# Kernel tuning notes

Measured on AMD Instinct MI355X. Metric: run time of the kernel, lower is better.

Reference implementation:

```python
import jax, jax.numpy as jnp
import numpy as np

D = 64        # dense voxel grid extent per axis
C = 256       # planes
R = 128       # planes // reduction
N = 100000    # number of occupied (unique) sparse voxels
K = 7         # max-pool kernel size
PAD = 3       # (K-1)//2, stride-1 'same' window


def setup_inputs() -> dict:
    key = jax.random.key(0)
    k1, k2, k3, k4 = jax.random.split(key, 4)
    feats = jax.random.normal(k1, (N, C), dtype=jnp.float32)
    # unique sparse coordinates in [0, D)^3 (MinkowskiEngine coords are unique)
    lin = jax.random.permutation(k2, D * D * D)[:N]
    coords = jnp.stack(jnp.unravel_index(lin, (D, D, D)), axis=-1).astype(jnp.int32)
    # 1x1 sparse convs == per-point linear layers (ME default bias=False)
    W1 = jax.random.normal(k3, (C, R), dtype=jnp.float32) * (1.0 / np.sqrt(C))
    W2 = jax.random.normal(k4, (R, C), dtype=jnp.float32) * (1.0 / np.sqrt(R))
    return {"feats": feats, "coords": coords, "W1": W1, "W2": W2}


def reference(feats, coords, W1, W2):
    neg_inf = jnp.array(-jnp.inf, dtype=feats.dtype)
    ix, iy, iz = coords[:, 0], coords[:, 1], coords[:, 2]
    # scatter sparse features into a dense grid; empty voxels = -inf so they
    grid = jnp.full((D, D, D, C), neg_inf, dtype=feats.dtype).at[ix, iy, iz].set(feats)
    # MinkowskiMaxPooling(kernel_size=7, stride=1): max over [-3,3]^3 window
    pooled = jax.lax.reduce_window(
        grid, neg_inf, jax.lax.max,
        window_dimensions=(K, K, K, 1),
        window_strides=(1, 1, 1, 1),
        padding=[(PAD, PAD), (PAD, PAD), (PAD, PAD), (0, 0)],
    )
    y = pooled[ix, iy, iz]  # [N, C], gather back to sparse points
    # fc: 1x1 conv -> ReLU -> 1x1 conv -> sigmoid (per-point MLP)
    y = jax.nn.sigmoid(jax.nn.relu(y @ W1) @ W2)
    return feats * y
```

## Files before the change

### kernel.cpp

```cpp
#include <hip/hip_runtime.h>
#include <hip/hip_bf16.h>

#define GD 64
#define GC 256

typedef unsigned short u16;
typedef unsigned int u32;
typedef short bf16x8 __attribute__((ext_vector_type(8)));
typedef float f32x4 __attribute__((ext_vector_type(4)));

__device__ __forceinline__ u16 f2bf_rne(float f) {
    u32 u = __builtin_bit_cast(u32, f);
    u = (u + 0x7FFFu + ((u >> 16) & 1u)) >> 16;
    return (u16)u;
}

__global__ __launch_bounds__(256) void init_grid(uint4* __restrict__ g, int n16) {
    int i = blockIdx.x * 256 + threadIdx.x;
    if (i < n16) {
        uint4 v;
        v.x = v.y = v.z = v.w = 0xFF80FF80u;
        g[i] = v;
    }
}

__global__ __launch_bounds__(256) void scatter_feats(const float* __restrict__ feats,
        const int* __restrict__ coords, u16* __restrict__ grid, int n) {
    int t = blockIdx.x * 256 + threadIdx.x;
    int i = t >> 5;
    if (i >= n) return;
    int c8 = (t & 31) << 3;
    int ix = coords[3 * i], iy = coords[3 * i + 1], iz = coords[3 * i + 2];
    size_t cell = (size_t)((ix * GD + iy) * GD + iz);
    const float4* src = (const float4*)(feats + (size_t)i * GC + c8);
    float4 a = src[0], b = src[1];
    u32 p0 = (u32)f2bf_rne(a.x) | ((u32)f2bf_rne(a.y) << 16);
    u32 p1 = (u32)f2bf_rne(a.z) | ((u32)f2bf_rne(a.w) << 16);
    u32 p2 = (u32)f2bf_rne(b.x) | ((u32)f2bf_rne(b.y) << 16);
    u32 p3 = (u32)f2bf_rne(b.z) | ((u32)f2bf_rne(b.w) << 16);
    uint4 v = make_uint4(p0, p1, p2, p3);
    *(uint4*)(grid + cell * GC + c8) = v;
}

__global__ __launch_bounds__(256) void prep_weights(const float* __restrict__ W1,
        const float* __restrict__ W2, u16* __restrict__ img1, u16* __restrict__ img2) {
    int t = blockIdx.x * 256 + threadIdx.x;
    if (t < 32768) {
        int h = t >> 14, nn = (t >> 8) & 63, chunk = (t >> 3) & 31, j = t & 7;
        int k = chunk * 8 + j;
        img1[(h << 14) + nn * 256 + (((chunk ^ (nn & 7)) << 3) | j)] =
            f2bf_rne(W1[k * 128 + h * 64 + nn]);
    } else {
        int t2 = t - 32768;
        int h = t2 >> 14, nn = (t2 >> 7) & 127, chunk = (t2 >> 3) & 15, j = t2 & 7;
        int k = chunk * 8 + j;
        img2[(h << 14) + nn * 128 + (((chunk ^ (nn & 7)) << 3) | j)] =
            f2bf_rne(W2[k * 256 + h * 128 + nn]);
    }
}

__device__ __forceinline__ void unpack8(uint4 r, float* w) {
    u32 v[4] = {r.x, r.y, r.z, r.w};
#pragma unroll
    for (int i = 0; i < 4; i++) {
        w[2 * i]     = __builtin_bit_cast(float, v[i] << 16);
        w[2 * i + 1] = __builtin_bit_cast(float, v[i] & 0xFFFF0000u);
    }
}

__global__ __launch_bounds__(256) void pool_pass_v(u16* __restrict__ grid,
        int mulA, int mulB, int strideCell) {
    int chunk = threadIdx.x & 31;
    int L = blockIdx.x * 8 + (threadIdx.x >> 5);
    int a = L >> 6, b = L & 63;
    size_t baseEl = ((size_t)a * mulA + (size_t)b * mulB) * GC + chunk * 8;
    size_t stepEl = (size_t)strideCell * GC;
    u16* p = grid + baseEl;

    float win[7][8];
#pragma unroll
    for (int s = 0; s < 7; s++)
#pragma unroll
        for (int c = 0; c < 8; c++) win[s][c] = -INFINITY;

#pragma unroll
    for (int t = 0; t < 3; t++) {
        uint4 r = *(const uint4*)(p + (size_t)t * stepEl);
        unpack8(r, win[t + 3]);
    }

#pragma unroll
    for (int z = 0; z < 64; z++) {
        int slot = (z + 6) % 7;
        if (z + 3 < 64) {
            uint4 r = *(const uint4*)(p + (size_t)(z + 3) * stepEl);
            unpack8(r, win[slot]);
        } else {
#pragma unroll
            for (int c = 0; c < 8; c++) win[slot][c] = -INFINITY;
        }
        u32 q[4];
#pragma unroll
        for (int i = 0; i < 4; i++) {
            u32 halves[2];
#pragma unroll
            for (int hh = 0; hh < 2; hh++) {
                int c = 2 * i + hh;
                float m01 = fmaxf(win[0][c], win[1][c]);
                float m23 = fmaxf(win[2][c], win[3][c]);
                float m45 = fmaxf(win[4][c], win[5][c]);
                float m = fmaxf(fmaxf(m01, m23), fmaxf(m45, win[6][c]));
                halves[hh] = __builtin_bit_cast(u32, m);
            }
            q[i] = (halves[0] >> 16) | (halves[1] & 0xFFFF0000u);
        }
        *(uint4*)(p + (size_t)z * stepEl) = make_uint4(q[0], q[1], q[2], q[3]);
    }
}

__global__ __launch_bounds__(256, 4) void gemm1_kernel(const u16* __restrict__ grid,
        const int* __restrict__ coords, const u16* __restrict__ img1,
        u16* __restrict__ H, int n, int nrb) {
    __shared__ __align__(16) u16 w1t[64 * 256];
    int h = blockIdx.x >= nrb;
    int rb = blockIdx.x - (h ? nrb : 0);
    int tid = threadIdx.x;

    const uint4* src = (const uint4*)(img1 + (h << 14));
    uint4* dst = (uint4*)w1t;
#pragma unroll
    for (int i = 0; i < 8; i++) dst[i * 256 + tid] = src[i * 256 + tid];

    int wave = tid >> 6, lane = tid & 63, m16 = lane & 15, quad = lane >> 4;
    int row_a = rb * 64 + wave * 16 + m16;
    int ra = min(row_a, n - 1);
    int ix = coords[3 * ra], iy = coords[3 * ra + 1], iz = coords[3 * ra + 2];
    const u16* yrow = grid + (size_t)((ix * GD + iy) * GD + iz) * GC;
    bf16x8 afr[8];
#pragma unroll
    for (int kk = 0; kk < 8; kk++)
        afr[kk] = *(const bf16x8*)(yrow + kk * 32 + quad * 8);
    __syncthreads();

    f32x4 acc[4];
#pragma unroll
    for (int t = 0; t < 4; t++) acc[t] = (f32x4){0.f, 0.f, 0.f, 0.f};
#pragma unroll
    for (int kk = 0; kk < 8; kk++) {
        int chunk = kk * 4 + quad;
#pragma unroll
        for (int t = 0; t < 4; t++) {
            int r = t * 16 + m16;
            bf16x8 b = *(const bf16x8*)&w1t[r * 256 + ((chunk ^ (r & 7)) << 3)];
            acc[t] = __builtin_amdgcn_mfma_f32_16x16x32_bf16(afr[kk], b, acc[t], 0, 0, 0);
        }
    }
    __syncthreads();

    u16* hbuf = w1t;
#pragma unroll
    for (int t = 0; t < 4; t++) {
        int col = t * 16 + m16;
        int c8 = col >> 3, j = col & 7;
#pragma unroll
        for (int rr = 0; rr < 4; rr++) {
            int row_l = wave * 16 + quad * 4 + rr;
            float hv = fmaxf(acc[t][rr], 0.0f);
            hbuf[row_l * 64 + (((c8 ^ (row_l & 7)) << 3) | j)] = f2bf_rne(hv);
        }
    }
    __syncthreads();
#pragma unroll
    for (int i = 0; i < 2; i++) {
        int cid = i * 256 + tid;
        int row_l = cid >> 3, c8 = cid & 7;
        int grow = rb * 64 + row_l;
        if (grow < n) {
            bf16x8 v = *(const bf16x8*)&hbuf[row_l * 64 + ((c8 ^ (row_l & 7)) << 3)];
            *(bf16x8*)&H[(size_t)grow * 128 + h * 64 + c8 * 8] = v;
        }
    }
}

__global__ __launch_bounds__(256, 4) void gemm2_kernel(const u16* __restrict__ H,
        const u16* __restrict__ img2, const float* __restrict__ feats,
        float* __restrict__ out, int n, int nrb) {
    __shared__ __align__(16) char smem[64 * 140 * 4];
    u16* w2t = (u16*)smem;
    float* zbuf = (float*)smem;
    int h = blockIdx.x >= nrb;
    int rb = blockIdx.x - (h ? nrb : 0);
    int tid = threadIdx.x;

    const uint4* src = (const uint4*)(img2 + (h << 14));
    uint4* dst = (uint4*)w2t;
#pragma unroll
    for (int i = 0; i < 8; i++) dst[i * 256 + tid] = src[i * 256 + tid];

    int wave = tid >> 6, lane = tid & 63, m16 = lane & 15, quad = lane >> 4;
    int row_a = rb * 64 + wave * 16 + m16;
    int ra = min(row_a, n - 1);
    const u16* hrow = H + (size_t)ra * 128;
    bf16x8 afr[4];
#pragma unroll
    for (int kk = 0; kk < 4; kk++)
        afr[kk] = *(const bf16x8*)(hrow + kk * 32 + quad * 8);
    __syncthreads();

    f32x4 acc[8];
#pragma unroll
    for (int t = 0; t < 8; t++) acc[t] = (f32x4){0.f, 0.f, 0.f, 0.f};
#pragma unroll
    for (int kk = 0; kk < 4; kk++) {
        int chunk = kk * 4 + quad;
#pragma unroll
        for (int t = 0; t < 8; t++) {
            int nn = t * 16 + m16;
            bf16x8 b = *(const bf16x8*)&w2t[nn * 128 + ((chunk ^ (nn & 7)) << 3)];
            acc[t] = __builtin_amdgcn_mfma_f32_16x16x32_bf16(afr[kk], b, acc[t], 0, 0, 0);
        }
    }
    __syncthreads();

#pragma unroll
    for (int t = 0; t < 8; t++) {
        int col = t * 16 + m16;
#pragma unroll
        for (int rr = 0; rr < 4; rr++) {
            int row_l = wave * 16 + quad * 4 + rr;
            zbuf[row_l * 140 + col] = acc[t][rr];
        }
    }
    __syncthreads();
#pragma unroll
    for (int i = 0; i < 8; i++) {
        int f = i * 256 + tid;
        int row_l = f >> 5, c4 = f & 31;
        int grow = rb * 64 + row_l;
        if (grow < n) {
            f32x4 z = *(const f32x4*)&zbuf[row_l * 140 + c4 * 4];
            size_t o = (size_t)grow * 256 + h * 128 + c4 * 4;
            f32x4 ft = *(const f32x4*)&feats[o];
            f32x4 r;
#pragma unroll
            for (int c = 0; c < 4; c++)
                r[c] = ft[c] / (1.0f + __expf(-z[c]));
            *(f32x4*)&out[o] = r;
        }
    }
}

extern "C" void kernel_launch(void* const* d_in, const int* in_sizes, int n_in,
                              void* d_out, int out_size, void* d_ws, size_t ws_size,
                              hipStream_t stream) {
    const float* feats = (const float*)d_in[0];
    const int* coords = (const int*)d_in[1];
    const float* W1 = (const float*)d_in[2];
    const float* W2 = (const float*)d_in[3];
    float* out = (float*)d_out;

    int n = in_sizes[1] / 3;

    size_t grid_bytes = (size_t)GD * GD * GD * GC * 2;
    u16* grid = (u16*)d_ws;
    u16* H = (u16*)((char*)d_ws + grid_bytes);
    u16* img1 = (u16*)((char*)d_ws + grid_bytes + (size_t)n * 128 * 2);
    u16* img2 = img1 + 32768;

    int n16 = (int)(grid_bytes / 16);
    init_grid<<<n16 / 256, 256, 0, stream>>>((uint4*)d_ws, n16);

    prep_weights<<<256, 256, 0, stream>>>(W1, W2, img1, img2);

    scatter_feats<<<(n * 32 + 255) / 256, 256, 0, stream>>>(feats, coords, grid, n);

    pool_pass_v<<<512, 256, 0, stream>>>(grid, GD * GD, GD, 1);
    pool_pass_v<<<512, 256, 0, stream>>>(grid, GD * GD, 1, GD);
    pool_pass_v<<<512, 256, 0, stream>>>(grid, GD, 1, GD * GD);

    int nrb = (n + 63) / 64;
    gemm1_kernel<<<2 * nrb, 256, 0, stream>>>(grid, coords, img1, H, n, nrb);
    gemm2_kernel<<<2 * nrb, 256, 0, stream>>>(H, img2, feats, out, n, nrb);
}
```

Measured before the change: 380.8 us.

## Replace dense grid init with occupancy map and fuse z/y pooling passes

Drops the full 134MB grid fill by tracking occupancy in an int map (-1 empty) and skipping reads of empty cells during the z pass. The z and y pooling passes are fused into one kernel that does the z sliding window in registers and the y window through a double-buffered shared tile. The final x pass writes pooled rows only for occupied cells into a compact per-point buffer, so gemm1 reads contiguously instead of gathering through coords. The cost is an extra map buffer and a block barrier per z step.

```diff
diff --git a/kernel.cpp b/kernel.cpp
--- a/kernel.cpp
+++ b/kernel.cpp
@@ -15,31 +15,168 @@
     return (u16)u;
 }
 
-__global__ __launch_bounds__(256) void init_grid(uint4* __restrict__ g, int n16) {
+__device__ __forceinline__ void unpack8(uint4 r, float* w) {
+    u32 v[4] = {r.x, r.y, r.z, r.w};
+#pragma unroll
+    for (int i = 0; i < 4; i++) {
+        w[2 * i]     = __builtin_bit_cast(float, v[i] << 16);
+        w[2 * i + 1] = __builtin_bit_cast(float, v[i] & 0xFFFF0000u);
+    }
+}
+
+__global__ __launch_bounds__(256) void init_map(uint4* __restrict__ m) {
     int i = blockIdx.x * 256 + threadIdx.x;
-    if (i < n16) {
-        uint4 v;
-        v.x = v.y = v.z = v.w = 0xFF80FF80u;
-        g[i] = v;
-    }
+    uint4 v;
+    v.x = v.y = v.z = v.w = 0xFFFFFFFFu;
+    m[i] = v;
 }
 
 __global__ __launch_bounds__(256) void scatter_feats(const float* __restrict__ feats,
-        const int* __restrict__ coords, u16* __restrict__ grid, int n) {
+        const int* __restrict__ coords, u16* __restrict__ grid,
+        int* __restrict__ map, int n) {
     int t = blockIdx.x * 256 + threadIdx.x;
     int i = t >> 5;
     if (i >= n) return;
     int c8 = (t & 31) << 3;
     int ix = coords[3 * i], iy = coords[3 * i + 1], iz = coords[3 * i + 2];
-    size_t cell = (size_t)((ix * GD + iy) * GD + iz);
+    int cell = (ix * GD + iy) * GD + iz;
+    if ((t & 31) == 0) map[cell] = i;
     const float4* src = (const float4*)(feats + (size_t)i * GC + c8);
     float4 a = src[0], b = src[1];
     u32 p0 = (u32)f2bf_rne(a.x) | ((u32)f2bf_rne(a.y) << 16);
     u32 p1 = (u32)f2bf_rne(a.z) | ((u32)f2bf_rne(a.w) << 16);
     u32 p2 = (u32)f2bf_rne(b.x) | ((u32)f2bf_rne(b.y) << 16);
     u32 p3 = (u32)f2bf_rne(b.z) | ((u32)f2bf_rne(b.w) << 16);
-    uint4 v = make_uint4(p0, p1, p2, p3);
-    *(uint4*)(grid + cell * GC + c8) = v;
+    *(uint4*)(grid + (size_t)cell * GC + c8) = make_uint4(p0, p1, p2, p3);
+}
+
+__global__ __launch_bounds__(512) void pool_zy(u16* __restrict__ grid,
+        const int* __restrict__ map) {
+    int x = blockIdx.x >> 2, cg = blockIdx.x & 3;
+    int y = threadIdx.x >> 3, c = threadIdx.x & 7;
+    int chunk = cg * 8 + c;
+    const int* mrow = map + (x * GD + y) * GD;
+    u16* p = grid + (size_t)((x * GD + y) * GD) * GC + chunk * 8;
+
+    __shared__ __align__(16) u16 zp[2][64][8][8];
+
+    float win[7][8];
+#pragma unroll
+    for (int s = 0; s < 7; s++)
+#pragma unroll
+        for (int cc = 0; cc < 8; cc++) win[s][cc] = -INFINITY;
+
+#pragma unroll
+    for (int t = 0; t < 3; t++) {
+        if (mrow[t] >= 0) {
+            uint4 r = *(const uint4*)(p + (size_t)t * GC);
+            unpack8(r, win[t + 3]);
+        }
+    }
+
+#pragma unroll
+    for (int z = 0; z < 64; z++) {
+        int slot = (z + 6) % 7;
+        if (z + 3 < 64 && mrow[z + 3] >= 0) {
+            uint4 r = *(const uint4*)(p + (size_t)(z + 3) * GC);
+            unpack8(r, win[slot]);
+        } else {
+#pragma unroll
+            for (int cc = 0; cc < 8; cc++) win[slot][cc] = -INFINITY;
+        }
+
+        float mz[8];
+#pragma unroll
+        for (int cc = 0; cc < 8; cc++) {
+            float m01 = fmaxf(win[0][cc], win[1][cc]);
+            float m23 = fmaxf(win[2][cc], win[3][cc]);
+            float m45 = fmaxf(win[4][cc], win[5][cc]);
+            mz[cc] = fmaxf(fmaxf(m01, m23), fmaxf(m45, win[6][cc]));
+        }
+        u32 q[4];
+#pragma unroll
+        for (int iq = 0; iq < 4; iq++) {
+            u32 h0 = __builtin_bit_cast(u32, mz[2 * iq]);
+            u32 h1 = __builtin_bit_cast(u32, mz[2 * iq + 1]);
+            q[iq] = (h0 >> 16) | (h1 & 0xFFFF0000u);
+        }
+        *(uint4*)&zp[z & 1][y][c][0] = make_uint4(q[0], q[1], q[2], q[3]);
+        __syncthreads();
+
+#pragma unroll
+        for (int dy = -3; dy <= 3; dy++) {
+            if (dy == 0) continue;
+            int yy = y + dy;
+            if (yy >= 0 && yy < 64) {
+                uint4 r = *(const uint4*)&zp[z & 1][yy][c][0];
+                float w[8];
+                unpack8(r, w);
+#pragma unroll
+                for (int cc = 0; cc < 8; cc++) mz[cc] = fmaxf(mz[cc], w[cc]);
+            }
+        }
+        u32 o[4];
+#pragma unroll
+        for (int iq = 0; iq < 4; iq++) {
+            u32 h0 = __builtin_bit_cast(u32, mz[2 * iq]);
+            u32 h1 = __builtin_bit_cast(u32, mz[2 * iq + 1]);
+            o[iq] = (h0 >> 16) | (h1 & 0xFFFF0000u);
+        }
+        *(uint4*)(p + (size_t)z * GC) = make_uint4(o[0], o[1], o[2], o[3]);
+    }
+}
+
+__global__ __launch_bounds__(256) void pool_x_compact(const u16* __restrict__ grid,
+        const int* __restrict__ map, u16* __restrict__ P) {
+    int chunk = threadIdx.x & 31;
+    int L = blockIdx.x * 8 + (threadIdx.x >> 5);
+    int y = L >> 6, z = L & 63;
+    int cellBase = y * GD + z;
+    const u16* p = grid + (size_t)cellBase * GC + chunk * 8;
+    size_t stepEl = (size_t)(GD * GD) * GC;
+
+    float win[7][8];
+#pragma unroll
+    for (int s = 0; s < 7; s++)
+#pragma unroll
+        for (int cc = 0; cc < 8; cc++) win[s][cc] = -INFINITY;
+
+#pragma unroll
+    for (int t = 0; t < 3; t++) {
+        uint4 r = *(const uint4*)(p + (size_t)t * stepEl);
+        unpack8(r, win[t + 3]);
+    }
+
+#pragma unroll
+    for (int x = 0; x < 64; x++) {
+        int slot = (x + 6) % 7;
+        if (x + 3 < 64) {
+            uint4 r = *(const uint4*)(p + (size_t)(x + 3) * stepEl);
+            unpack8(r, win[slot]);
+        } else {
+#pragma unroll
+            for (int cc = 0; cc < 8; cc++) win[slot][cc] = -INFINITY;
+        }
+        int mi = map[cellBase + x * GD * GD];
+        if (mi >= 0) {
+            u32 q[4];
+#pragma unroll
+            for (int iq = 0; iq < 4; iq++) {
+                u32 halves[2];
+#pragma unroll
+                for (int hh = 0; hh < 2; hh++) {
+                    int cc = 2 * iq + hh;
+                    float m01 = fmaxf(win[0][cc], win[1][cc]);
+                    float m23 = fmaxf(win[2][cc], win[3][cc]);
+                    float m45 = fmaxf(win[4][cc], win[5][cc]);
+                    float m = fmaxf(fmaxf(m01, m23), fmaxf(m45, win[6][cc]));
+                    halves[hh] = __builtin_bit_cast(u32, m);
+                }
+                q[iq] = (halves[0] >> 16) | (halves[1] & 0xFFFF0000u);
+            }
+            *(uint4*)(P + (size_t)mi * GC + chunk * 8) = make_uint4(q[0], q[1], q[2], q[3]);
+        }
+    }
 }
 
 __global__ __launch_bounds__(256) void prep_weights(const float* __restrict__ W1,
@@ -59,68 +196,8 @@
     }
 }
 
-__device__ __forceinline__ void unpack8(uint4 r, float* w) {
-    u32 v[4] = {r.x, r.y, r.z, r.w};
-#pragma unroll
-    for (int i = 0; i < 4; i++) {
-        w[2 * i]     = __builtin_bit_cast(float, v[i] << 16);
-        w[2 * i + 1] = __builtin_bit_cast(float, v[i] & 0xFFFF0000u);
-    }
-}
-
-__global__ __launch_bounds__(256) void pool_pass_v(u16* __restrict__ grid,
-        int mulA, int mulB, int strideCell) {
-    int chunk = threadIdx.x & 31;
-    int L = blockIdx.x * 8 + (threadIdx.x >> 5);
-    int a = L >> 6, b = L & 63;
-    size_t baseEl = ((size_t)a * mulA + (size_t)b * mulB) * GC + chunk * 8;
-    size_t stepEl = (size_t)strideCell * GC;
-    u16* p = grid + baseEl;
-
-    float win[7][8];
-#pragma unroll
-    for (int s = 0; s < 7; s++)
-#pragma unroll
-        for (int c = 0; c < 8; c++) win[s][c] = -INFINITY;
-
-#pragma unroll
-    for (int t = 0; t < 3; t++) {
-        uint4 r = *(const uint4*)(p + (size_t)t * stepEl);
-        unpack8(r, win[t + 3]);
-    }
-
-#pragma unroll
-    for (int z = 0; z < 64; z++) {
-        int slot = (z + 6) % 7;
-        if (z + 3 < 64) {
-            uint4 r = *(const uint4*)(p + (size_t)(z + 3) * stepEl);
-            unpack8(r, win[slot]);
-        } else {
-#pragma unroll
-            for (int c = 0; c < 8; c++) win[slot][c] = -INFINITY;
-        }
-        u32 q[4];
-#pragma unroll
-        for (int i = 0; i < 4; i++) {
-            u32 halves[2];
-#pragma unroll
-            for (int hh = 0; hh < 2; hh++) {
-                int c = 2 * i + hh;
-                float m01 = fmaxf(win[0][c], win[1][c]);
-                float m23 = fmaxf(win[2][c], win[3][c]);
-                float m45 = fmaxf(win[4][c], win[5][c]);
-                float m = fmaxf(fmaxf(m01, m23), fmaxf(m45, win[6][c]));
-                halves[hh] = __builtin_bit_cast(u32, m);
-            }
-            q[i] = (halves[0] >> 16) | (halves[1] & 0xFFFF0000u);
-        }
-        *(uint4*)(p + (size_t)z * stepEl) = make_uint4(q[0], q[1], q[2], q[3]);
-    }
-}
-
-__global__ __launch_bounds__(256, 4) void gemm1_kernel(const u16* __restrict__ grid,
-        const int* __restrict__ coords, const u16* __restrict__ img1,
-        u16* __restrict__ H, int n, int nrb) {
+__global__ __launch_bounds__(256, 4) void gemm1_kernel(const u16* __restrict__ P,
+        const u16* __restrict__ img1, u16* __restrict__ H, int n, int nrb) {
     __shared__ __align__(16) u16 w1t[64 * 256];
     int h = blockIdx.x >= nrb;
     int rb = blockIdx.x - (h ? nrb : 0);
@@ -134,8 +211,7 @@
     int wave = tid >> 6, lane = tid & 63, m16 = lane & 15, quad = lane >> 4;
     int row_a = rb * 64 + wave * 16 + m16;
     int ra = min(row_a, n - 1);
-    int ix = coords[3 * ra], iy = coords[3 * ra + 1], iz = coords[3 * ra + 2];
-    const u16* yrow = grid + (size_t)((ix * GD + iy) * GD + iz) * GC;
+    const u16* yrow = P + (size_t)ra * GC;
     bf16x8 afr[8];
 #pragma unroll
     for (int kk = 0; kk < 8; kk++)
@@ -262,23 +338,23 @@
     int n = in_sizes[1] / 3;
 
     size_t grid_bytes = (size_t)GD * GD * GD * GC * 2;
+    size_t P_bytes = (size_t)n * GC * 2;
+    size_t H_bytes = (size_t)n * 128 * 2;
     u16* grid = (u16*)d_ws;
-    u16* H = (u16*)((char*)d_ws + grid_bytes);
-    u16* img1 = (u16*)((char*)d_ws + grid_bytes + (size_t)n * 128 * 2);
+    u16* P = (u16*)((char*)d_ws + grid_bytes);
+    u16* H = (u16*)((char*)d_ws + grid_bytes + P_bytes);
+    int* map = (int*)((char*)d_ws + grid_bytes + P_bytes + H_bytes);
+    u16* img1 = (u16*)((char*)map + (size_t)GD * GD * GD * 4);
     u16* img2 = img1 + 32768;
 
-    int n16 = (int)(grid_bytes / 16);
-    init_grid<<<n16 / 256, 256, 0, stream>>>((uint4*)d_ws, n16);
-
+    init_map<<<256, 256, 0, stream>>>((uint4*)map);
     prep_weights<<<256, 256, 0, stream>>>(W1, W2, img1, img2);
-
-    scatter_feats<<<(n * 32 + 255) / 256, 256, 0, stream>>>(feats, coords, grid, n);
-
-    pool_pass_v<<<512, 256, 0, stream>>>(grid, GD * GD, GD, 1);
-    pool_pass_v<<<512, 256, 0, stream>>>(grid, GD * GD, 1, GD);
-    pool_pass_v<<<512, 256, 0, stream>>>(grid, GD, 1, GD * GD);
+    scatter_feats<<<(n * 32 + 255) / 256, 256, 0, stream>>>(feats, coords, grid, map, n);
+
+    pool_zy<<<256, 512, 0, stream>>>(grid, map);
+    pool_x_compact<<<512, 256, 0, stream>>>(grid, map, P);
 
     int nrb = (n + 63) / 64;
-    gemm1_kernel<<<2 * nrb, 256, 0, stream>>>(grid, coords, img1, H, n, nrb);
+    gemm1_kernel<<<2 * nrb, 256, 0, stream>>>(P, img1, H, n, nrb);
     gemm2_kernel<<<2 * nrb, 256, 0, stream>>>(H, img2, feats, out, n, nrb);
 }
```

After: 623.1 us. 63.6% more time.

## Replace dense grid init and scatter with index map; fuse gather and compaction into pool passes

Applied to the files above, without the earlier changes.

Drops the dense grid fill and the feature scatter. A 64^3 index map is built instead, and the first pooling pass (z) reads features straight through that map. The y pass goes out-of-place into a second grid, and the x pass writes results only for occupied voxels into a compact [N,C] buffer that gemm1 reads contiguously. Each pooling thread now computes 4 outputs from a 10-wide window with high parallelism, where before each thread walked a 64-long serial sweep. This removes a full-grid memory write and the scattered gather, at the cost of doubling workspace usage.

```diff
diff --git a/kernel.cpp b/kernel.cpp
--- a/kernel.cpp
+++ b/kernel.cpp
@@ -15,31 +15,191 @@
     return (u16)u;
 }
 
-__global__ __launch_bounds__(256) void init_grid(uint4* __restrict__ g, int n16) {
+__device__ __forceinline__ float bfval(float f) {
+    u32 u = __builtin_bit_cast(u32, f);
+    u = (u + 0x7FFFu + ((u >> 16) & 1u)) & 0xFFFF0000u;
+    return __builtin_bit_cast(float, u);
+}
+
+__device__ __forceinline__ void unpack8(uint4 r, float* w) {
+    u32 v[4] = {r.x, r.y, r.z, r.w};
+#pragma unroll
+    for (int i = 0; i < 4; i++) {
+        w[2 * i]     = __builtin_bit_cast(float, v[i] << 16);
+        w[2 * i + 1] = __builtin_bit_cast(float, v[i] & 0xFFFF0000u);
+    }
+}
+
+__global__ __launch_bounds__(256) void init_map(uint4* __restrict__ m) {
     int i = blockIdx.x * 256 + threadIdx.x;
-    if (i < n16) {
-        uint4 v;
-        v.x = v.y = v.z = v.w = 0xFF80FF80u;
-        g[i] = v;
-    }
-}
-
-__global__ __launch_bounds__(256) void scatter_feats(const float* __restrict__ feats,
-        const int* __restrict__ coords, u16* __restrict__ grid, int n) {
-    int t = blockIdx.x * 256 + threadIdx.x;
-    int i = t >> 5;
-    if (i >= n) return;
-    int c8 = (t & 31) << 3;
-    int ix = coords[3 * i], iy = coords[3 * i + 1], iz = coords[3 * i + 2];
-    size_t cell = (size_t)((ix * GD + iy) * GD + iz);
-    const float4* src = (const float4*)(feats + (size_t)i * GC + c8);
-    float4 a = src[0], b = src[1];
-    u32 p0 = (u32)f2bf_rne(a.x) | ((u32)f2bf_rne(a.y) << 16);
-    u32 p1 = (u32)f2bf_rne(a.z) | ((u32)f2bf_rne(a.w) << 16);
-    u32 p2 = (u32)f2bf_rne(b.x) | ((u32)f2bf_rne(b.y) << 16);
-    u32 p3 = (u32)f2bf_rne(b.z) | ((u32)f2bf_rne(b.w) << 16);
-    uint4 v = make_uint4(p0, p1, p2, p3);
-    *(uint4*)(grid + cell * GC + c8) = v;
+    uint4 v;
+    v.x = v.y = v.z = v.w = 0xFFFFFFFFu;
+    m[i] = v;
+}
+
+__global__ __launch_bounds__(256) void build_map(const int* __restrict__ coords,
+        int* __restrict__ map, int n) {
+    int i = blockIdx.x * 256 + threadIdx.x;
+    if (i < n) {
+        int ix = coords[3 * i], iy = coords[3 * i + 1], iz = coords[3 * i + 2];
+        map[(ix * GD + iy) * GD + iz] = i;
+    }
+}
+
+__device__ __forceinline__ void max4pack(const float (&v)[10][8], u32 (&q)[4][4]) {
+#pragma unroll
+    for (int i = 0; i < 4; i++) {
+        u32 h[4][2];
+#pragma unroll
+        for (int hh = 0; hh < 2; hh++) {
+            int ch = 2 * i + hh;
+            float p0 = fmaxf(v[0][ch], v[1][ch]);
+            float p2 = fmaxf(v[2][ch], v[3][ch]);
+            float p4 = fmaxf(v[4][ch], v[5][ch]);
+            float p6 = fmaxf(v[6][ch], v[7][ch]);
+            float p8 = fmaxf(v[8][ch], v[9][ch]);
+            float o0 = fmaxf(fmaxf(p0, p2), fmaxf(p4, v[6][ch]));
+            float o1 = fmaxf(fmaxf(v[1][ch], p2), fmaxf(p4, p6));
+            float o2 = fmaxf(fmaxf(p2, p4), fmaxf(p6, v[8][ch]));
+            float o3 = fmaxf(fmaxf(v[3][ch], p4), fmaxf(p6, p8));
+            h[0][hh] = __builtin_bit_cast(u32, o0);
+            h[1][hh] = __builtin_bit_cast(u32, o1);
+            h[2][hh] = __builtin_bit_cast(u32, o2);
+            h[3][hh] = __builtin_bit_cast(u32, o3);
+        }
+#pragma unroll
+        for (int d = 0; d < 4; d++)
+            q[d][i] = (h[d][0] >> 16) | (h[d][1] & 0xFFFF0000u);
+    }
+}
+
+__global__ __launch_bounds__(256, 3) void pool_z_gather(const float* __restrict__ feats,
+        const int* __restrict__ map, u16* __restrict__ grid) {
+    int lane = threadIdx.x & 31;
+    int gid = blockIdx.x * 8 + (threadIdx.x >> 5);
+    int L = gid >> 4;
+    int a0 = (gid & 15) << 2;
+    const int* mrow = map + L * GD;
+    const float* fb = feats + lane * 8;
+    u16* po = grid + ((size_t)L * GD + a0) * GC + lane * 8;
+
+    int mi[10];
+#pragma unroll
+    for (int i = 0; i < 10; i++) {
+        int w = a0 - 3 + i;
+        int wc = min(max(w, 0), 63);
+        int m = mrow[wc];
+        mi[i] = ((unsigned)w < 64u) ? m : -1;
+    }
+
+    float4 fa[10], fbb[10];
+#pragma unroll
+    for (int i = 0; i < 10; i++) {
+        const float4* f4 = (const float4*)(fb + (size_t)max(mi[i], 0) * GC);
+        fa[i] = f4[0];
+        fbb[i] = f4[1];
+    }
+    asm volatile("" ::: "memory");
+
+    float v[10][8];
+#pragma unroll
+    for (int i = 0; i < 10; i++) {
+        bool s = mi[i] >= 0;
+        v[i][0] = bfval(s ? fa[i].x : -INFINITY);
+        v[i][1] = bfval(s ? fa[i].y : -INFINITY);
+        v[i][2] = bfval(s ? fa[i].z : -INFINITY);
+        v[i][3] = bfval(s ? fa[i].w : -INFINITY);
+        v[i][4] = bfval(s ? fbb[i].x : -INFINITY);
+        v[i][5] = bfval(s ? fbb[i].y : -INFINITY);
+        v[i][6] = bfval(s ? fbb[i].z : -INFINITY);
+        v[i][7] = bfval(s ? fbb[i].w : -INFINITY);
+    }
+
+    u32 q[4][4];
+    max4pack(v, q);
+#pragma unroll
+    for (int d = 0; d < 4; d++)
+        *(uint4*)(po + (size_t)d * GC) = make_uint4(q[d][0], q[d][1], q[d][2], q[d][3]);
+}
+
+__global__ __launch_bounds__(256, 3) void pool_y(const u16* __restrict__ gin,
+        u16* __restrict__ gout) {
+    int lane = threadIdx.x & 31;
+    int gid = blockIdx.x * 8 + (threadIdx.x >> 5);
+    int L = gid >> 4;
+    int a0 = (gid & 15) << 2;
+    int x = L >> 6, z = L & 63;
+    size_t base = ((size_t)x * GD * GD + z) * GC + lane * 8;
+    const size_t st = (size_t)GD * GC;
+    const u16* pin = gin + base;
+    u16* po = gout + base + (size_t)a0 * st;
+
+    uint4 c[10];
+#pragma unroll
+    for (int i = 0; i < 10; i++) {
+        int wc = min(max(a0 - 3 + i, 0), 63);
+        c[i] = *(const uint4*)(pin + (size_t)wc * st);
+    }
+    asm volatile("" ::: "memory");
+
+    float v[10][8];
+#pragma unroll
+    for (int i = 0; i < 10; i++) {
+        float t[8];
+        unpack8(c[i], t);
+        bool ok = (unsigned)(a0 - 3 + i) < 64u;
+#pragma unroll
+        for (int ch = 0; ch < 8; ch++) v[i][ch] = ok ? t[ch] : -INFINITY;
+    }
+
+    u32 q[4][4];
+    max4pack(v, q);
+#pragma unroll
+    for (int d = 0; d < 4; d++)
+        *(uint4*)(po + (size_t)d * st) = make_uint4(q[d][0], q[d][1], q[d][2], q[d][3]);
+}
+
+__global__ __launch_bounds__(256, 3) void pool_x_compact(const u16* __restrict__ gin,
+        const int* __restrict__ map, u16* __restrict__ P) {
+    int lane = threadIdx.x & 31;
+    int gid = blockIdx.x * 8 + (threadIdx.x >> 5);
+    int L = gid >> 4;
+    int a0 = (gid & 15) << 2;
+    size_t base = (size_t)L * GC + lane * 8;
+    const size_t st = (size_t)GD * GD * GC;
+    const u16* pin = gin + base;
+
+    int mo[4];
+#pragma unroll
+    for (int d = 0; d < 4; d++)
+        mo[d] = map[(size_t)(a0 + d) * GD * GD + L];
+
+    uint4 c[10];
+#pragma unroll
+    for (int i = 0; i < 10; i++) {
+        int wc = min(max(a0 - 3 + i, 0), 63);
+        c[i] = *(const uint4*)(pin + (size_t)wc * st);
+    }
+    asm volatile("" ::: "memory");
+
+    float v[10][8];
+#pragma unroll
+    for (int i = 0; i < 10; i++) {
+        float t[8];
+        unpack8(c[i], t);
+        bool ok = (unsigned)(a0 - 3 + i) < 64u;
+#pragma unroll
+        for (int ch = 0; ch < 8; ch++) v[i][ch] = ok ? t[ch] : -INFINITY;
+    }
+
+    u32 q[4][4];
+    max4pack(v, q);
+#pragma unroll
+    for (int d = 0; d < 4; d++) {
+        if (mo[d] >= 0)
+            *(uint4*)(P + (size_t)mo[d] * GC + lane * 8) =
+                make_uint4(q[d][0], q[d][1], q[d][2], q[d][3]);
+    }
 }
 
 __global__ __launch_bounds__(256) void prep_weights(const float* __restrict__ W1,
@@ -59,68 +219,8 @@
     }
 }
 
-__device__ __forceinline__ void unpack8(uint4 r, float* w) {
-    u32 v[4] = {r.x, r.y, r.z, r.w};
-#pragma unroll
-    for (int i = 0; i < 4; i++) {
-        w[2 * i]     = __builtin_bit_cast(float, v[i] << 16);
-        w[2 * i + 1] = __builtin_bit_cast(float, v[i] & 0xFFFF0000u);
-    }
-}
-
-__global__ __launch_bounds__(256) void pool_pass_v(u16* __restrict__ grid,
-        int mulA, int mulB, int strideCell) {
-    int chunk = threadIdx.x & 31;
-    int L = blockIdx.x * 8 + (threadIdx.x >> 5);
-    int a = L >> 6, b = L & 63;
-    size_t baseEl = ((size_t)a * mulA + (size_t)b * mulB) * GC + chunk * 8;
-    size_t stepEl = (size_t)strideCell * GC;
-    u16* p = grid + baseEl;
-
-    float win[7][8];
-#pragma unroll
-    for (int s = 0; s < 7; s++)
-#pragma unroll
-        for (int c = 0; c < 8; c++) win[s][c] = -INFINITY;
-
-#pragma unroll
-    for (int t = 0; t < 3; t++) {
-        uint4 r = *(const uint4*)(p + (size_t)t * stepEl);
-        unpack8(r, win[t + 3]);
-    }
-
-#pragma unroll
-    for (int z = 0; z < 64; z++) {
-        int slot = (z + 6) % 7;
-        if (z + 3 < 64) {
-            uint4 r = *(const uint4*)(p + (size_t)(z + 3) * stepEl);
-            unpack8(r, win[slot]);
-        } else {
-#pragma unroll
-            for (int c = 0; c < 8; c++) win[slot][c] = -INFINITY;
-        }
-        u32 q[4];
-#pragma unroll
-        for (int i = 0; i < 4; i++) {
-            u32 halves[2];
-#pragma unroll
-            for (int hh = 0; hh < 2; hh++) {
-                int c = 2 * i + hh;
-                float m01 = fmaxf(win[0][c], win[1][c]);
-                float m23 = fmaxf(win[2][c], win[3][c]);
-                float m45 = fmaxf(win[4][c], win[5][c]);
-                float m = fmaxf(fmaxf(m01, m23), fmaxf(m45, win[6][c]));
-                halves[hh] = __builtin_bit_cast(u32, m);
-            }
-            q[i] = (halves[0] >> 16) | (halves[1] & 0xFFFF0000u);
-        }
-        *(uint4*)(p + (size_t)z * stepEl) = make_uint4(q[0], q[1], q[2], q[3]);
-    }
-}
-
-__global__ __launch_bounds__(256, 4) void gemm1_kernel(const u16* __restrict__ grid,
-        const int* __restrict__ coords, const u16* __restrict__ img1,
-        u16* __restrict__ H, int n, int nrb) {
+__global__ __launch_bounds__(256, 4) void gemm1_kernel(const u16* __restrict__ P,
+        const u16* __restrict__ img1, u16* __restrict__ H, int n, int nrb) {
     __shared__ __align__(16) u16 w1t[64 * 256];
     int h = blockIdx.x >= nrb;
     int rb = blockIdx.x - (h ? nrb : 0);
@@ -134,8 +234,7 @@
     int wave = tid >> 6, lane = tid & 63, m16 = lane & 15, quad = lane >> 4;
     int row_a = rb * 64 + wave * 16 + m16;
     int ra = min(row_a, n - 1);
-    int ix = coords[3 * ra], iy = coords[3 * ra + 1], iz = coords[3 * ra + 2];
-    const u16* yrow = grid + (size_t)((ix * GD + iy) * GD + iz) * GC;
+    const u16* yrow = P + (size_t)ra * GC;
     bf16x8 afr[8];
 #pragma unroll
     for (int kk = 0; kk < 8; kk++)
@@ -262,23 +361,25 @@
     int n = in_sizes[1] / 3;
 
     size_t grid_bytes = (size_t)GD * GD * GD * GC * 2;
+    size_t P_bytes = (size_t)n * GC * 2;
+    size_t H_bytes = (size_t)n * 128 * 2;
     u16* grid = (u16*)d_ws;
-    u16* H = (u16*)((char*)d_ws + grid_bytes);
-    u16* img1 = (u16*)((char*)d_ws + grid_bytes + (size_t)n * 128 * 2);
+    u16* grid2 = (u16*)((char*)d_ws + grid_bytes);
+    u16* P = (u16*)((char*)d_ws + 2 * grid_bytes);
+    u16* H = (u16*)((char*)d_ws + 2 * grid_bytes + P_bytes);
+    int* map = (int*)((char*)d_ws + 2 * grid_bytes + P_bytes + H_bytes);
+    u16* img1 = (u16*)((char*)map + (size_t)GD * GD * GD * 4);
     u16* img2 = img1 + 32768;
 
-    int n16 = (int)(grid_bytes / 16);
-    init_grid<<<n16 / 256, 256, 0, stream>>>((uint4*)d_ws, n16);
-
+    init_map<<<256, 256, 0, stream>>>((uint4*)map);
     prep_weights<<<256, 256, 0, stream>>>(W1, W2, img1, img2);
-
-    scatter_feats<<<(n * 32 + 255) / 256, 256, 0, stream>>>(feats, coords, grid, n);
-
-    pool_pass_v<<<512, 256, 0, stream>>>(grid, GD * GD, GD, 1);
-    pool_pass_v<<<512, 256, 0, stream>>>(grid, GD * GD, 1, GD);
-    pool_pass_v<<<512, 256, 0, stream>>>(grid, GD, 1, GD * GD);
+    build_map<<<(n + 255) / 256, 256, 0, stream>>>(coords, map, n);
+
+    pool_z_gather<<<8192, 256, 0, stream>>>(feats, map, grid);
+    pool_y<<<8192, 256, 0, stream>>>(grid, grid2);
+    pool_x_compact<<<8192, 256, 0, stream>>>(grid2, map, P);
 
     int nrb = (n + 63) / 64;
-    gemm1_kernel<<<2 * nrb, 256, 0, stream>>>(grid, coords, img1, H, n, nrb);
+    gemm1_kernel<<<2 * nrb, 256, 0, stream>>>(P, img1, H, n, nrb);
     gemm2_kernel<<<2 * nrb, 256, 0, stream>>>(H, img2, feats, out, n, nrb);
 }
```

After: 381.0 us. About the same (+0.0%).
